# Kernel optimization log

Hardware: AMD Instinct MI355X
Metric: run time of the kernel (lower is better)

The kernel has to match this reference:

```python
import jax, jax.numpy as jnp
import numpy as np
import math

N, C, H, W = 4, 256, 64, 64
CH = C // 2  # theta/phi output channels


def setup_inputs() -> dict:
    key = jax.random.key(0)
    k1, k2, k3 = jax.random.split(key, 3)
    x = jax.random.normal(k1, (N, C, H, W), dtype=jnp.float32)
    # 1x1 conv weights, init normal(0, 0.01) as in reset_params
    theta_w = 0.01 * jax.random.normal(k2, (CH, C), dtype=jnp.float32)
    phi_w = 0.01 * jax.random.normal(k3, (CH, C), dtype=jnp.float32)
    theta_b = jnp.zeros((CH,), dtype=jnp.float32)
    phi_b = jnp.zeros((CH,), dtype=jnp.float32)
    return {"x": x, "theta_w": theta_w, "theta_b": theta_b, "phi_w": phi_w, "phi_b": phi_b}


def reference(x, theta_w, theta_b, phi_w, phi_b):
    n, c, h, w = x.shape
    hw = h * w
    scale = 1.0 / math.sqrt(c)  # divide by sqrt(self.in_ch)
    # 1x1 convs (pointwise channel mixes)
    q = jnp.einsum('nchw,dc->ndhw', x, theta_w) + theta_b[None, :, None, None]
    k = jnp.einsum('nchw,dc->ndhw', x, phi_w) + phi_b[None, :, None, None]
    # affinity: [n, hw, hw] (flattened 'nabcd' tensor)
    q2 = q.reshape(n, c // 2, hw)
    k2 = k.reshape(n, c // 2, hw)
    ff = jnp.einsum('nis,nit->nst', q2, k2) * scale
    attn = jax.nn.softmax(ff, axis=-1)
    # weighted sum of values x: out[n,i,s] = sum_t attn[n,s,t] x[n,i,t]
    out = jnp.einsum('nst,nit->nis', attn, x.reshape(n, c, hw))
    return out.reshape(x.shape)
```

## Files before the change

### kernel.cpp

```cpp
#include <hip/hip_runtime.h>

#define S_LEN 4096
#define C_CH  256
#define D_CH  128
#define LAMBDA 0.09016844005555896f

typedef __attribute__((ext_vector_type(8)))  short short8;
typedef __attribute__((ext_vector_type(4)))  float f32x4;
typedef __attribute__((ext_vector_type(16))) float f32x16;

union PFrag { unsigned u[4]; short8 v; };

static __device__ __forceinline__ unsigned short f2bf(float x) {
    union { float f; unsigned u; } v; v.f = x;
    unsigned r = v.u + 0x7FFFu + ((v.u >> 16) & 1u);
    return (unsigned short)(r >> 16);
}

static __device__ __forceinline__ void gload_lds16(const void* g, void* l) {
    __builtin_amdgcn_global_load_lds(
        (const __attribute__((address_space(1))) void*)g,
        (__attribute__((address_space(3))) void*)l, 16, 0, 0);
}

__global__ void nlm_conv_kernel(const float* __restrict__ x, unsigned short* __restrict__ xb) {
    size_t base = ((size_t)blockIdx.x * 256 + threadIdx.x) * 4;
    float4 v = *reinterpret_cast<const float4*>(x + base);
    ushort4 b; b.x = f2bf(v.x); b.y = f2bf(v.y); b.z = f2bf(v.z); b.w = f2bf(v.w);
    *reinterpret_cast<ushort4*>(xb + base) = b;
}

__global__ void nlm_wconv_kernel(const float* __restrict__ tw, const float* __restrict__ pw,
                                 unsigned short* __restrict__ wb) {
    int base = (blockIdx.x * 256 + threadIdx.x) * 4;
    const float* src = (base < 32768) ? (tw + base) : (pw + base - 32768);
    float4 v = *reinterpret_cast<const float4*>(src);
    ushort4 b; b.x = f2bf(v.x); b.y = f2bf(v.y); b.z = f2bf(v.z); b.w = f2bf(v.w);
    *reinterpret_cast<ushort4*>(wb + base) = b;
}

__launch_bounds__(256, 1)
__global__ void nlm_proj_kernel(const float* __restrict__ x,
                                const unsigned short* __restrict__ wb,
                                const float* __restrict__ tb, const float* __restrict__ pbias,
                                unsigned short* __restrict__ Qb, unsigned short* __restrict__ Kb) {
    const int n    = blockIdx.y;
    const int wave = threadIdx.x >> 6;
    const int lane = threadIdx.x & 63;
    const int sl   = lane & 15, g = lane >> 4;
    const int s0   = blockIdx.x * 64 + wave * 16;
    const float* xn = x + (size_t)n * C_CH * S_LEN;

    f32x4 acc[16];
    #pragma unroll
    for (int i = 0; i < 16; ++i) acc[i] = (f32x4){0.f, 0.f, 0.f, 0.f};

    #pragma unroll 1
    for (int cc = 0; cc < 8; ++cc) {
        short8 af;
        #pragma unroll
        for (int j = 0; j < 8; ++j) {
            float v = xn[(size_t)(cc * 32 + g * 8 + j) * S_LEN + s0 + sl];
            af[j] = (short)f2bf(v);
        }
        #pragma unroll
        for (int t = 0; t < 16; ++t) {
            const unsigned short* wp = wb + (size_t)(t >> 3) * (D_CH * C_CH)
                                          + (size_t)((t & 7) * 16 + sl) * C_CH + cc * 32 + g * 8;
            short8 bf = *reinterpret_cast<const short8*>(wp);
            acc[t] = __builtin_amdgcn_mfma_f32_16x16x32_bf16(af, bf, acc[t], 0, 0, 0);
        }
    }
    unsigned short* Qn = Qb + (size_t)n * S_LEN * D_CH;
    unsigned short* Kn = Kb + (size_t)n * S_LEN * D_CH;
    #pragma unroll
    for (int t = 0; t < 16; ++t) {
        const float bias = (t < 8 ? tb : pbias)[(t & 7) * 16 + sl];
        unsigned short* dst = (t < 8 ? Qn : Kn);
        #pragma unroll
        for (int r = 0; r < 4; ++r) {
            float val = acc[t][r] + bias;
            if (t < 8) val *= LAMBDA;
            dst[(size_t)(s0 + g * 4 + r) * D_CH + (t & 7) * 16 + sl] = f2bf(val);
        }
    }
}

template<int TSPLIT>
__launch_bounds__(512, 2)
__global__ void nlm_attn_kernel(const unsigned short* __restrict__ Qb,
                                const unsigned short* __restrict__ Kb,
                                const unsigned short* __restrict__ xb,
                                float* __restrict__ part0, float* __restrict__ part1,
                                float* __restrict__ part2, float* __restrict__ part3,
                                float* __restrict__ lbuf) {
    constexpr int TRANGE = S_LEN / TSPLIT;
    constexpr int NITv   = TRANGE / 64;
    constexpr int TOTAL  = 64 * TSPLIT;
    const int sid  = blockIdx.x;
    const int newb = (sid & 7) * (TOTAL / 8) + (sid >> 3);
    const int n    = newb / (16 * TSPLIT);
    const int th   = (newb >> 4) & (TSPLIT - 1);
    const int sb   = newb & 15;
    const int lane = threadIdx.x & 63;
    const int wave = threadIdx.x >> 6;
    const int l31  = lane & 31;
    const int h    = lane >> 5;
    const int s0   = sb * 256 + wave * 32;
    const int tbase = th * TRANGE;

    __shared__ unsigned short Klds[2][64 * 128];
    __shared__ unsigned short Vlds[2][256 * 64];

    const unsigned short* Qn = Qb + (size_t)n * S_LEN * D_CH;
    const unsigned short* Kn = Kb + (size_t)n * S_LEN * D_CH;
    const unsigned short* xn = xb + (size_t)n * C_CH * S_LEN;

    short8 qf[8];
    #pragma unroll
    for (int ks = 0; ks < 8; ++ks)
        qf[ks] = *reinterpret_cast<const short8*>(Qn + (size_t)(s0 + l31) * D_CH + ks * 16 + h * 8);

    f32x16 oacc[8];
    #pragma unroll
    for (int i = 0; i < 8; ++i)
        #pragma unroll
        for (int r = 0; r < 16; ++r) oacc[i][r] = 0.f;
    float lsum = 0.f;

    auto kstage = [&](int itv, int slot) {
        const int it = itv < NITv ? itv : NITv - 1;
        const int t0 = tbase + it * 64;
        #pragma unroll
        for (int i = 0; i < 2; ++i) {
            const int rl = wave * 8 + i * 4 + (lane >> 4);
            const int ch = (lane & 15) ^ (rl & 7);
            gload_lds16(Kn + (size_t)(t0 + rl) * D_CH + ch * 8,
                        &Klds[slot][(wave * 8 + i * 4) * 128]);
        }
    };
    auto vstage = [&](int itv, int slot) {
        const int it = itv < NITv ? itv : NITv - 1;
        const int t0 = tbase + it * 64;
        #pragma unroll
        for (int i = 0; i < 4; ++i) {
            const int row = wave * 32 + i * 8 + (lane >> 3);
            const int ch = (lane & 7) ^ (row & 7);
            gload_lds16(xn + (size_t)row * S_LEN + t0 + ch * 8,
                        &Vlds[slot][(wave * 32 + i * 8) * 64]);
        }
    };

    kstage(0, 0); vstage(0, 0);
    asm volatile("s_waitcnt vmcnt(0)" ::: "memory");

    #pragma unroll 1
    for (int it = 0; it < NITv; ++it) {
        const int cur = it & 1;
        __builtin_amdgcn_s_barrier();
        __builtin_amdgcn_sched_barrier(0);
        kstage(it + 1, cur ^ 1);
        vstage(it + 1, cur ^ 1);

        f32x16 sa, sb2;
        #pragma unroll
        for (int r = 0; r < 16; ++r) { sa[r] = 0.f; sb2[r] = 0.f; }
        __builtin_amdgcn_s_setprio(1);
        #pragma unroll
        for (int ks = 0; ks < 8; ++ks) {
            const int ch = (ks * 2 + h) ^ (l31 & 7);
            short8 kflo = *reinterpret_cast<const short8*>(&Klds[cur][l31 * 128 + ch * 8]);
            short8 kfhi = *reinterpret_cast<const short8*>(&Klds[cur][(32 + l31) * 128 + ch * 8]);
            sa  = __builtin_amdgcn_mfma_f32_32x32x16_bf16(kflo, qf[ks], sa,  0, 0, 0);
            sb2 = __builtin_amdgcn_mfma_f32_32x32x16_bf16(kfhi, qf[ks], sb2, 0, 0, 0);
        }
        __builtin_amdgcn_s_setprio(0);

        PFrag pa0, pa1, pa2, pa3;
        float rs = 0.f;
        {
            float p[16];
            #pragma unroll
            for (int r = 0; r < 16; ++r) { p[r] = __builtin_amdgcn_exp2f(sa[r]); rs += p[r]; }
            unsigned W0, W1, W2, W3, W4, W5, W6, W7;
            asm("v_cvt_pk_bf16_f32 %0, %1, %2" : "=v"(W0) : "v"(p[0]),  "v"(p[1]));
            asm("v_cvt_pk_bf16_f32 %0, %1, %2" : "=v"(W1) : "v"(p[2]),  "v"(p[3]));
            asm("v_cvt_pk_bf16_f32 %0, %1, %2" : "=v"(W2) : "v"(p[4]),  "v"(p[5]));
            asm("v_cvt_pk_bf16_f32 %0, %1, %2" : "=v"(W3) : "v"(p[6]),  "v"(p[7]));
            asm("v_cvt_pk_bf16_f32 %0, %1, %2" : "=v"(W4) : "v"(p[8]),  "v"(p[9]));
            asm("v_cvt_pk_bf16_f32 %0, %1, %2" : "=v"(W5) : "v"(p[10]), "v"(p[11]));
            asm("v_cvt_pk_bf16_f32 %0, %1, %2" : "=v"(W6) : "v"(p[12]), "v"(p[13]));
            asm("v_cvt_pk_bf16_f32 %0, %1, %2" : "=v"(W7) : "v"(p[14]), "v"(p[15]));
            asm("v_permlane32_swap_b32 %0, %1" : "+v"(W0), "+v"(W2));
            asm("v_permlane32_swap_b32 %0, %1" : "+v"(W1), "+v"(W3));
            asm("v_permlane32_swap_b32 %0, %1" : "+v"(W4), "+v"(W6));
            asm("v_permlane32_swap_b32 %0, %1" : "+v"(W5), "+v"(W7));
            pa0.u[0] = W0; pa0.u[1] = W1; pa0.u[2] = W2; pa0.u[3] = W3;
            pa1.u[0] = W4; pa1.u[1] = W5; pa1.u[2] = W6; pa1.u[3] = W7;
        }
        {
            float p[16];
            #pragma unroll
            for (int r = 0; r < 16; ++r) { p[r] = __builtin_amdgcn_exp2f(sb2[r]); rs += p[r]; }
            unsigned W0, W1, W2, W3, W4, W5, W6, W7;
            asm("v_cvt_pk_bf16_f32 %0, %1, %2" : "=v"(W0) : "v"(p[0]),  "v"(p[1]));
            asm("v_cvt_pk_bf16_f32 %0, %1, %2" : "=v"(W1) : "v"(p[2]),  "v"(p[3]));
            asm("v_cvt_pk_bf16_f32 %0, %1, %2" : "=v"(W2) : "v"(p[4]),  "v"(p[5]));
            asm("v_cvt_pk_bf16_f32 %0, %1, %2" : "=v"(W3) : "v"(p[6]),  "v"(p[7]));
            asm("v_cvt_pk_bf16_f32 %0, %1, %2" : "=v"(W4) : "v"(p[8]),  "v"(p[9]));
            asm("v_cvt_pk_bf16_f32 %0, %1, %2" : "=v"(W5) : "v"(p[10]), "v"(p[11]));
            asm("v_cvt_pk_bf16_f32 %0, %1, %2" : "=v"(W6) : "v"(p[12]), "v"(p[13]));
            asm("v_cvt_pk_bf16_f32 %0, %1, %2" : "=v"(W7) : "v"(p[14]), "v"(p[15]));
            asm("v_permlane32_swap_b32 %0, %1" : "+v"(W0), "+v"(W2));
            asm("v_permlane32_swap_b32 %0, %1" : "+v"(W1), "+v"(W3));
            asm("v_permlane32_swap_b32 %0, %1" : "+v"(W4), "+v"(W6));
            asm("v_permlane32_swap_b32 %0, %1" : "+v"(W5), "+v"(W7));
            pa2.u[0] = W0; pa2.u[1] = W1; pa2.u[2] = W2; pa2.u[3] = W3;
            pa3.u[0] = W4; pa3.u[1] = W5; pa3.u[2] = W6; pa3.u[3] = W7;
        }
        lsum += rs;

        __builtin_amdgcn_s_setprio(1);
        #pragma unroll
        for (int cb = 0; cb < 8; ++cb) {
            const int c = cb * 32 + l31;
            const unsigned short* Vr = &Vlds[cur][c * 64];
            const int f = l31 & 7;
            short8 vf0 = *reinterpret_cast<const short8*>(&Vr[((0 + h) ^ f) * 8]);
            short8 vf1 = *reinterpret_cast<const short8*>(&Vr[((2 + h) ^ f) * 8]);
            short8 vf2 = *reinterpret_cast<const short8*>(&Vr[((4 + h) ^ f) * 8]);
            short8 vf3 = *reinterpret_cast<const short8*>(&Vr[((6 + h) ^ f) * 8]);
            oacc[cb] = __builtin_amdgcn_mfma_f32_32x32x16_bf16(vf0, pa0.v, oacc[cb], 0, 0, 0);
            oacc[cb] = __builtin_amdgcn_mfma_f32_32x32x16_bf16(vf1, pa1.v, oacc[cb], 0, 0, 0);
            oacc[cb] = __builtin_amdgcn_mfma_f32_32x32x16_bf16(vf2, pa2.v, oacc[cb], 0, 0, 0);
            oacc[cb] = __builtin_amdgcn_mfma_f32_32x32x16_bf16(vf3, pa3.v, oacc[cb], 0, 0, 0);
        }
        __builtin_amdgcn_s_setprio(0);

        asm volatile("s_waitcnt vmcnt(0)" ::: "memory");
        __builtin_amdgcn_sched_barrier(0);
    }

    float lt = lsum + __shfl_xor(lsum, 32);
    float* dst = (th == 0) ? part0 : (th == 1) ? part1 : (th == 2) ? part2 : part3;
    if (lane < 32) lbuf[th * 16384 + n * 4096 + s0 + lane] = lt;
    float* on = dst + (size_t)n * C_CH * S_LEN;
    #pragma unroll
    for (int cb = 0; cb < 8; ++cb) {
        #pragma unroll
        for (int r = 0; r < 16; ++r) {
            const int c = cb * 32 + (r & 3) + 8 * (r >> 2) + 4 * h;
            on[(size_t)c * S_LEN + s0 + l31] = oacc[cb][r];
        }
    }
}

template<int TSPLIT>
__global__ void nlm_combine_kernel(float* __restrict__ out, const float* __restrict__ p1,
                                   const float* __restrict__ p2, const float* __restrict__ p3,
                                   const float* __restrict__ lbuf) {
    const size_t e0 = ((size_t)blockIdx.x * 256 + threadIdx.x) * 4;
    const int n = (int)(e0 >> 20);
    const int s = (int)(e0 & 4095);
    float4 o = *reinterpret_cast<const float4*>(out + e0);
    float4 l = *reinterpret_cast<const float4*>(lbuf + n * 4096 + s);
    {
        float4 ov = *reinterpret_cast<const float4*>(p1 + e0);
        float4 lv = *reinterpret_cast<const float4*>(lbuf + 16384 + n * 4096 + s);
        o.x += ov.x; o.y += ov.y; o.z += ov.z; o.w += ov.w;
        l.x += lv.x; l.y += lv.y; l.z += lv.z; l.w += lv.w;
    }
    if (TSPLIT == 4) {
        float4 ov = *reinterpret_cast<const float4*>(p2 + e0);
        float4 lv = *reinterpret_cast<const float4*>(lbuf + 2 * 16384 + n * 4096 + s);
        o.x += ov.x; o.y += ov.y; o.z += ov.z; o.w += ov.w;
        l.x += lv.x; l.y += lv.y; l.z += lv.z; l.w += lv.w;
        float4 ow = *reinterpret_cast<const float4*>(p3 + e0);
        float4 lw = *reinterpret_cast<const float4*>(lbuf + 3 * 16384 + n * 4096 + s);
        o.x += ow.x; o.y += ow.y; o.z += ow.z; o.w += ow.w;
        l.x += lw.x; l.y += lw.y; l.z += lw.z; l.w += lw.w;
    }
    float4 r;
    r.x = o.x / l.x; r.y = o.y / l.y; r.z = o.z / l.z; r.w = o.w / l.w;
    *reinterpret_cast<float4*>(out + e0) = r;
}

extern "C" void kernel_launch(void* const* d_in, const int* in_sizes, int n_in,
                              void* d_out, int out_size, void* d_ws, size_t ws_size,
                              hipStream_t stream) {
    const float* x  = (const float*)d_in[0];
    const float* tw = (const float*)d_in[1];
    const float* tb = (const float*)d_in[2];
    const float* pw = (const float*)d_in[3];
    const float* pb = (const float*)d_in[4];
    float* out = (float*)d_out;

    char* ws = (char*)d_ws;
    unsigned short* xb = (unsigned short*)(ws);
    unsigned short* Qb = (unsigned short*)(ws + 8388608);
    unsigned short* Kb = (unsigned short*)(ws + 12582912);
    unsigned short* wb = (unsigned short*)(ws + 16777216);
    float*          lb = (float*)(ws + 16908288);
    float*          p1 = (float*)(ws + 17825792);
    float*          p2 = (float*)(ws + 34603008);
    float*          p3 = (float*)(ws + 51380224);

    nlm_conv_kernel<<<4096, 256, 0, stream>>>(x, xb);
    nlm_wconv_kernel<<<64, 256, 0, stream>>>(tw, pw, wb);
    nlm_proj_kernel<<<dim3(64, 4), 256, 0, stream>>>(x, wb, tb, pb, Qb, Kb);
    if (ws_size >= (size_t)68157440) {
        nlm_attn_kernel<4><<<256, 512, 0, stream>>>(Qb, Kb, xb, out, p1, p2, p3, lb);
        nlm_combine_kernel<4><<<4096, 256, 0, stream>>>(out, p1, p2, p3, lb);
    } else {
        nlm_attn_kernel<2><<<128, 512, 0, stream>>>(Qb, Kb, xb, out, p1, p1, p1, lb);
        nlm_combine_kernel<2><<<4096, 256, 0, stream>>>(out, p1, p1, p1, lb);
    }
}
```

Before: 100.7 us.

## Store Q/K in FP8 and use FP8 MFMA for the QK^T scores

The projection kernel now writes Q and K as FP8 instead of BF16, moving the softmax scale from the Q projection into the exponent in the attention loop. The attention kernel stages K in LDS as FP8 with an adjusted swizzle and computes scores with fp8 32x32x16 MFMA. This halves the Q/K memory traffic and LDS footprint for K and uses the cheaper FP8 matrix path. The cost is reduced precision in the attention logits, with only narrow byte stores in the projection epilogue.

```diff
diff --git a/kernel.cpp b/kernel.cpp
--- a/kernel.cpp
+++ b/kernel.cpp
@@ -43,7 +43,7 @@
 __global__ void nlm_proj_kernel(const float* __restrict__ x,
                                 const unsigned short* __restrict__ wb,
                                 const float* __restrict__ tb, const float* __restrict__ pbias,
-                                unsigned short* __restrict__ Qb, unsigned short* __restrict__ Kb) {
+                                unsigned char* __restrict__ Qb8, unsigned char* __restrict__ Kb8) {
     const int n    = blockIdx.y;
     const int wave = threadIdx.x >> 6;
     const int lane = threadIdx.x & 63;
@@ -71,25 +71,27 @@
             acc[t] = __builtin_amdgcn_mfma_f32_16x16x32_bf16(af, bf, acc[t], 0, 0, 0);
         }
     }
-    unsigned short* Qn = Qb + (size_t)n * S_LEN * D_CH;
-    unsigned short* Kn = Kb + (size_t)n * S_LEN * D_CH;
     #pragma unroll
     for (int t = 0; t < 16; ++t) {
         const float bias = (t < 8 ? tb : pbias)[(t & 7) * 16 + sl];
-        unsigned short* dst = (t < 8 ? Qn : Kn);
-        #pragma unroll
-        for (int r = 0; r < 4; ++r) {
-            float val = acc[t][r] + bias;
-            if (t < 8) val *= LAMBDA;
-            dst[(size_t)(s0 + g * 4 + r) * D_CH + (t & 7) * 16 + sl] = f2bf(val);
-        }
+        unsigned char* dst = (t < 8 ? Qb8 : Kb8) + (size_t)n * S_LEN * D_CH;
+        const int col = (t & 7) * 16 + sl;
+        float v0 = acc[t][0] + bias, v1 = acc[t][1] + bias;
+        float v2 = acc[t][2] + bias, v3 = acc[t][3] + bias;
+        unsigned u01, u23;
+        asm("v_cvt_pk_fp8_f32 %0, %1, %2" : "=v"(u01) : "v"(v0), "v"(v1));
+        asm("v_cvt_pk_fp8_f32 %0, %1, %2" : "=v"(u23) : "v"(v2), "v"(v3));
+        dst[(size_t)(s0 + g * 4 + 0) * D_CH + col] = (unsigned char)(u01 & 0xff);
+        dst[(size_t)(s0 + g * 4 + 1) * D_CH + col] = (unsigned char)((u01 >> 8) & 0xff);
+        dst[(size_t)(s0 + g * 4 + 2) * D_CH + col] = (unsigned char)(u23 & 0xff);
+        dst[(size_t)(s0 + g * 4 + 3) * D_CH + col] = (unsigned char)((u23 >> 8) & 0xff);
     }
 }
 
 template<int TSPLIT>
 __launch_bounds__(512, 2)
-__global__ void nlm_attn_kernel(const unsigned short* __restrict__ Qb,
-                                const unsigned short* __restrict__ Kb,
+__global__ void nlm_attn_kernel(const unsigned char* __restrict__ Qb8,
+                                const unsigned char* __restrict__ Kb8,
                                 const unsigned short* __restrict__ xb,
                                 float* __restrict__ part0, float* __restrict__ part1,
                                 float* __restrict__ part2, float* __restrict__ part3,
@@ -109,17 +111,17 @@
     const int s0   = sb * 256 + wave * 32;
     const int tbase = th * TRANGE;
 
-    __shared__ unsigned short Klds[2][64 * 128];
+    __shared__ unsigned char  Klds[2][64 * 128];
     __shared__ unsigned short Vlds[2][256 * 64];
 
-    const unsigned short* Qn = Qb + (size_t)n * S_LEN * D_CH;
-    const unsigned short* Kn = Kb + (size_t)n * S_LEN * D_CH;
+    const unsigned char* Qn8 = Qb8 + (size_t)n * S_LEN * D_CH;
+    const unsigned char* Kn8 = Kb8 + (size_t)n * S_LEN * D_CH;
     const unsigned short* xn = xb + (size_t)n * C_CH * S_LEN;
 
-    short8 qf[8];
+    long qf8[8];
     #pragma unroll
     for (int ks = 0; ks < 8; ++ks)
-        qf[ks] = *reinterpret_cast<const short8*>(Qn + (size_t)(s0 + l31) * D_CH + ks * 16 + h * 8);
+        qf8[ks] = *reinterpret_cast<const long*>(Qn8 + (size_t)(s0 + l31) * D_CH + ks * 16 + h * 8);
 
     f32x16 oacc[8];
     #pragma unroll
@@ -131,13 +133,10 @@
     auto kstage = [&](int itv, int slot) {
         const int it = itv < NITv ? itv : NITv - 1;
         const int t0 = tbase + it * 64;
-        #pragma unroll
-        for (int i = 0; i < 2; ++i) {
-            const int rl = wave * 8 + i * 4 + (lane >> 4);
-            const int ch = (lane & 15) ^ (rl & 7);
-            gload_lds16(Kn + (size_t)(t0 + rl) * D_CH + ch * 8,
-                        &Klds[slot][(wave * 8 + i * 4) * 128]);
-        }
+        const int rl = wave * 8 + (lane >> 3);
+        const int ch = (lane & 7) ^ (rl & 7);
+        gload_lds16(Kn8 + (size_t)(t0 + rl) * D_CH + ch * 16,
+                    &Klds[slot][wave * 8 * 128]);
     };
     auto vstage = [&](int itv, int slot) {
         const int it = itv < NITv ? itv : NITv - 1;
@@ -165,14 +164,15 @@
         f32x16 sa, sb2;
         #pragma unroll
         for (int r = 0; r < 16; ++r) { sa[r] = 0.f; sb2[r] = 0.f; }
+        const int f = l31 & 7;
         __builtin_amdgcn_s_setprio(1);
         #pragma unroll
         for (int ks = 0; ks < 8; ++ks) {
-            const int ch = (ks * 2 + h) ^ (l31 & 7);
-            short8 kflo = *reinterpret_cast<const short8*>(&Klds[cur][l31 * 128 + ch * 8]);
-            short8 kfhi = *reinterpret_cast<const short8*>(&Klds[cur][(32 + l31) * 128 + ch * 8]);
-            sa  = __builtin_amdgcn_mfma_f32_32x32x16_bf16(kflo, qf[ks], sa,  0, 0, 0);
-            sb2 = __builtin_amdgcn_mfma_f32_32x32x16_bf16(kfhi, qf[ks], sb2, 0, 0, 0);
+            const int co = ((ks ^ f) * 16) + h * 8;
+            long kflo = *reinterpret_cast<const long*>(&Klds[cur][l31 * 128 + co]);
+            long kfhi = *reinterpret_cast<const long*>(&Klds[cur][(32 + l31) * 128 + co]);
+            sa  = __builtin_amdgcn_mfma_f32_32x32x16_fp8_fp8(kflo, qf8[ks], sa,  0, 0, 0);
+            sb2 = __builtin_amdgcn_mfma_f32_32x32x16_fp8_fp8(kfhi, qf8[ks], sb2, 0, 0, 0);
         }
         __builtin_amdgcn_s_setprio(0);
 
@@ -181,7 +181,7 @@
         {
             float p[16];
             #pragma unroll
-            for (int r = 0; r < 16; ++r) { p[r] = __builtin_amdgcn_exp2f(sa[r]); rs += p[r]; }
+            for (int r = 0; r < 16; ++r) { p[r] = __builtin_amdgcn_exp2f(sa[r] * LAMBDA); rs += p[r]; }
             unsigned W0, W1, W2, W3, W4, W5, W6, W7;
             asm("v_cvt_pk_bf16_f32 %0, %1, %2" : "=v"(W0) : "v"(p[0]),  "v"(p[1]));
             asm("v_cvt_pk_bf16_f32 %0, %1, %2" : "=v"(W1) : "v"(p[2]),  "v"(p[3]));
@@ -201,7 +201,7 @@
         {
             float p[16];
             #pragma unroll
-            for (int r = 0; r < 16; ++r) { p[r] = __builtin_amdgcn_exp2f(sb2[r]); rs += p[r]; }
+            for (int r = 0; r < 16; ++r) { p[r] = __builtin_amdgcn_exp2f(sb2[r] * LAMBDA); rs += p[r]; }
             unsigned W0, W1, W2, W3, W4, W5, W6, W7;
             asm("v_cvt_pk_bf16_f32 %0, %1, %2" : "=v"(W0) : "v"(p[0]),  "v"(p[1]));
             asm("v_cvt_pk_bf16_f32 %0, %1, %2" : "=v"(W1) : "v"(p[2]),  "v"(p[3]));
@@ -225,11 +225,11 @@
         for (int cb = 0; cb < 8; ++cb) {
             const int c = cb * 32 + l31;
             const unsigned short* Vr = &Vlds[cur][c * 64];
-            const int f = l31 & 7;
-            short8 vf0 = *reinterpret_cast<const short8*>(&Vr[((0 + h) ^ f) * 8]);
-            short8 vf1 = *reinterpret_cast<const short8*>(&Vr[((2 + h) ^ f) * 8]);
-            short8 vf2 = *reinterpret_cast<const short8*>(&Vr[((4 + h) ^ f) * 8]);
-            short8 vf3 = *reinterpret_cast<const short8*>(&Vr[((6 + h) ^ f) * 8]);
+            const int fv = l31 & 7;
+            short8 vf0 = *reinterpret_cast<const short8*>(&Vr[((0 + h) ^ fv) * 8]);
+            short8 vf1 = *reinterpret_cast<const short8*>(&Vr[((2 + h) ^ fv) * 8]);
+            short8 vf2 = *reinterpret_cast<const short8*>(&Vr[((4 + h) ^ fv) * 8]);
+            short8 vf3 = *reinterpret_cast<const short8*>(&Vr[((6 + h) ^ fv) * 8]);
             oacc[cb] = __builtin_amdgcn_mfma_f32_32x32x16_bf16(vf0, pa0.v, oacc[cb], 0, 0, 0);
             oacc[cb] = __builtin_amdgcn_mfma_f32_32x32x16_bf16(vf1, pa1.v, oacc[cb], 0, 0, 0);
             oacc[cb] = __builtin_amdgcn_mfma_f32_32x32x16_bf16(vf2, pa2.v, oacc[cb], 0, 0, 0);
@@ -297,8 +297,8 @@
 
     char* ws = (char*)d_ws;
     unsigned short* xb = (unsigned short*)(ws);
-    unsigned short* Qb = (unsigned short*)(ws + 8388608);
-    unsigned short* Kb = (unsigned short*)(ws + 12582912);
+    unsigned char*  Qb8 = (unsigned char*)(ws + 8388608);
+    unsigned char*  Kb8 = (unsigned char*)(ws + 12582912);
     unsigned short* wb = (unsigned short*)(ws + 16777216);
     float*          lb = (float*)(ws + 16908288);
     float*          p1 = (float*)(ws + 17825792);
@@ -307,12 +307,12 @@
 
     nlm_conv_kernel<<<4096, 256, 0, stream>>>(x, xb);
     nlm_wconv_kernel<<<64, 256, 0, stream>>>(tw, pw, wb);
-    nlm_proj_kernel<<<dim3(64, 4), 256, 0, stream>>>(x, wb, tb, pb, Qb, Kb);
+    nlm_proj_kernel<<<dim3(64, 4), 256, 0, stream>>>(x, wb, tb, pb, Qb8, Kb8);
     if (ws_size >= (size_t)68157440) {
-        nlm_attn_kernel<4><<<256, 512, 0, stream>>>(Qb, Kb, xb, out, p1, p2, p3, lb);
+        nlm_attn_kernel<4><<<256, 512, 0, stream>>>(Qb8, Kb8, xb, out, p1, p2, p3, lb);
         nlm_combine_kernel<4><<<4096, 256, 0, stream>>>(out, p1, p2, p3, lb);
     } else {
-        nlm_attn_kernel<2><<<128, 512, 0, stream>>>(Qb, Kb, xb, out, p1, p1, p1, lb);
+        nlm_attn_kernel<2><<<128, 512, 0, stream>>>(Qb8, Kb8, xb, out, p1, p1, p1, lb);
         nlm_combine_kernel<2><<<4096, 256, 0, stream>>>(out, p1, p1, p1, lb);
     }
 }
```

Result: faster. 98.55 us (-2.2%).
